# Kernel tuning notes

Hardware: AMD Instinct MI355X
Metric: run time of the kernel (lower is better)

The kernel has to match this reference:

```python
import jax, jax.numpy as jnp
import numpy as np

A = -0.75  # torch bicubic coefficient
K = 5
K2 = K * K
IN_CH = 32 * 2 + 169 + 16 * 2 + 1  # 266
TIMESTEP = 0.5


def _cubic_w(t):
    # t in [0,1); weights for taps at offsets -1,0,1,2 (torch cubic convolution, A=-0.75)
    w1 = ((A + 2.0) * t - (A + 3.0)) * t * t + 1.0
    s = 1.0 - t
    w2 = ((A + 2.0) * s - (A + 3.0)) * s * s + 1.0
    u = t + 1.0
    w0 = ((A * u - 5.0 * A) * u + 8.0 * A) * u - 4.0 * A
    v = 2.0 - t
    w3 = ((A * v - 5.0 * A) * v + 8.0 * A) * v - 4.0 * A
    return (w0, w1, w2, w3)


def _conv3(x, w, b):
    y = jax.lax.conv_general_dilated(x, w, (1, 1), 'SAME',
                                     dimension_numbers=('NCHW', 'OIHW', 'NCHW'))
    return y + b[None, :, None, None]


def _lrelu(x):
    return jnp.where(x >= 0, x, 0.1 * x)


def _kernel_pred(x, w1, b1, w2, b2, w3, b3, ow, ob, ww, wb):
    f = _lrelu(_conv3(x, w1, b1))
    f = _lrelu(_conv3(f, w2, b2))
    f = _lrelu(_conv3(f, w3, b3))
    offsets = _conv3(f, ow, ob)                      # (B, 2*K2, H, W)
    weights = jax.nn.softmax(_conv3(f, ww, wb), axis=1)  # (B, K2, H, W)
    return offsets, weights


def _adacof_sample(image, offsets, weights):
    # bicubic grid_sample(padding_mode='border', align_corners=True) + weighted combine
    b, c, h, w = image.shape
    k2 = weights.shape[1]
    gx = jnp.arange(w, dtype=image.dtype)
    gy = jnp.arange(h, dtype=image.dtype)
    dx = offsets[:, 0::2]                # (b,k2,h,w)
    dy = offsets[:, 1::2]
    # with align_corners=True, normalize->unnormalize is identity
    sx = gx[None, None, None, :] + dx
    sy = gy[None, None, :, None] + dy
    x0 = jnp.floor(sx); tx = sx - x0
    y0 = jnp.floor(sy); ty = sy - y0
    wx = _cubic_w(tx)
    wy = _cubic_w(ty)
    xi = [jnp.clip(x0 + (i - 1.0), 0, w - 1).astype(jnp.int32) for i in range(4)]
    yi = [jnp.clip(y0 + (i - 1.0), 0, h - 1).astype(jnp.int32) for i in range(4)]
    imgf = image.reshape(b, c, h * w)
    gather = jax.vmap(lambda im, idx: im[:, idx])   # (c,hw),(n,)->(c,n)
    acc = jnp.zeros((b, c, k2, h, w), image.dtype)
    for i in range(4):
        for j in range(4):
            idx = (yi[i] * w + xi[j]).reshape(b, -1)
            g = gather(imgf, idx).reshape(b, c, k2, h, w)
            acc = acc + g * (wy[i] * wx[j])[:, None]
    return jnp.einsum('bckhw,bkhw->bchw', acc, weights)


def setup_inputs() -> dict:
    key = jax.random.key(0)
    ks = iter(jax.random.split(key, 64))
    d = {}
    d['frame1'] = jax.random.normal(next(ks), (2, 3, 256, 256), jnp.float32)
    d['frame2'] = jax.random.normal(next(ks), (2, 3, 256, 256), jnp.float32)
    d['feat1'] = jax.random.normal(next(ks), (2, 32, 256, 256), jnp.float32)
    d['feat2'] = jax.random.normal(next(ks), (2, 32, 256, 256), jnp.float32)
    d['corr'] = jax.random.normal(next(ks), (2, 169, 256, 256), jnp.float32)

    def conv_w(o, i):
        return jax.random.normal(next(ks), (o, i, 3, 3), jnp.float32) * 0.05

    # full-res encoder
    d['fr_w1'] = conv_w(16, 3); d['fr_b1'] = jnp.zeros((16,), jnp.float32)
    d['fr_w2'] = conv_w(16, 16); d['fr_b2'] = jnp.zeros((16,), jnp.float32)
    # default grid offsets for offset_head bias (dx,dy interleaved)
    off_bias = []
    for i in range(K):
        for j in range(K):
            off_bias.extend([j - K // 2, i - K // 2])
    off_bias = jnp.asarray(off_bias, jnp.float32)
    for p in ('kp1', 'kp2'):
        d[p + '_w1'] = conv_w(256, IN_CH); d[p + '_b1'] = jnp.zeros((256,), jnp.float32)
        d[p + '_w2'] = conv_w(256, 256); d[p + '_b2'] = jnp.zeros((256,), jnp.float32)
        d[p + '_w3'] = conv_w(128, 256); d[p + '_b3'] = jnp.zeros((128,), jnp.float32)
        d[p + '_ow'] = jax.random.normal(next(ks), (2 * K2, 128, 3, 3), jnp.float32) * 0.01
        d[p + '_ob'] = off_bias
        d[p + '_ww'] = jax.random.normal(next(ks), (K2, 128, 3, 3), jnp.float32) * 0.01
        d[p + '_wb'] = jnp.full((K2,), 1.0 / K2, jnp.float32)
    d['bl_w1'] = conv_w(64, IN_CH); d['bl_b1'] = jnp.zeros((64,), jnp.float32)
    d['bl_w2'] = conv_w(1, 64); d['bl_b2'] = jnp.zeros((1,), jnp.float32)
    return d


def reference(frame1, frame2, feat1, feat2, corr,
              fr_w1, fr_b1, fr_w2, fr_b2,
              kp1_w1, kp1_b1, kp1_w2, kp1_b2, kp1_w3, kp1_b3, kp1_ow, kp1_ob, kp1_ww, kp1_wb,
              kp2_w1, kp2_b1, kp2_w2, kp2_b2, kp2_w3, kp2_b3, kp2_ow, kp2_ob, kp2_ww, kp2_wb,
              bl_w1, bl_b1, bl_w2, bl_b2):
    b, _, h, w = frame1.shape
    fr1 = _lrelu(_conv3(_lrelu(_conv3(frame1, fr_w1, fr_b1)), fr_w2, fr_b2))
    fr2 = _lrelu(_conv3(_lrelu(_conv3(frame2, fr_w1, fr_b1)), fr_w2, fr_b2))
    t_map = jnp.full((b, 1, h, w), TIMESTEP, frame1.dtype)
    combined = jnp.concatenate([feat1, feat2, corr, fr1, fr2, t_map], axis=1)
    offsets1, weights1 = _kernel_pred(combined, kp1_w1, kp1_b1, kp1_w2, kp1_b2,
                                      kp1_w3, kp1_b3, kp1_ow, kp1_ob, kp1_ww, kp1_wb)
    offsets2, weights2 = _kernel_pred(combined, kp2_w1, kp2_b1, kp2_w2, kp2_b2,
                                      kp2_w3, kp2_b3, kp2_ow, kp2_ob, kp2_ww, kp2_wb)
    sample1 = _adacof_sample(frame1, offsets1, weights1)
    sample2 = _adacof_sample(frame2, offsets2, weights2)
    blend = jax.nn.sigmoid(_conv3(_lrelu(_conv3(combined, bl_w1, bl_b1)), bl_w2, bl_b2))
    output = blend * sample1 + (1.0 - blend) * sample2
    return (output, blend, offsets1, offsets2, weights1, weights2)
```

## Files before the change

kernel.cpp:

```cpp
#include <hip/hip_runtime.h>
#include <cstdint>
#include <cstddef>

#define H 256
#define W 256
#define HW (H*W)
#define BATCH 2
#define CIN_TILE 4

typedef __bf16 bf16x8 __attribute__((ext_vector_type(8)));
typedef float f32x4 __attribute__((ext_vector_type(4)));
typedef __attribute__((address_space(1))) uint32_t gu32_t;
typedef __attribute__((address_space(3))) uint32_t lu32_t;

__device__ __forceinline__ void async16(const void* g, void* l) {
  __builtin_amdgcn_global_load_lds((const gu32_t*)g, (lu32_t*)l, 16, 0, 0);
}

__device__ __forceinline__ ushort f2bf(float f) {
  uint u = __float_as_uint(f);
  return (ushort)((u + 0x7FFFu + ((u >> 16) & 1u)) >> 16);
}
__device__ __forceinline__ float lrelu_f(float v) { return v >= 0.f ? v : 0.1f * v; }

template<int EPI>
__global__ __launch_bounds__(256) void convmm_k(
    const ushort* __restrict__ act, const ushort* __restrict__ wgt,
    const float* __restrict__ bias, ushort* __restrict__ dstb,
    float* __restrict__ dsto, float* __restrict__ dstw,
    const ushort* __restrict__ zpage, int Cin, int CoutS,
    int astride, int wstride, int bstride, int dstride)
{
  const int z = blockIdx.z;
  act += (size_t)z * astride;
  wgt += (size_t)z * wstride;
  bias += (size_t)z * bstride;
  if constexpr (EPI == 0) dstb += (size_t)z * dstride;
  else { dsto += (size_t)z * (BATCH * 50 * HW); dstw += (size_t)z * (BATCH * 25 * HW); }

  __shared__ __align__(16) ushort s_w[2304 * 8];
  __shared__ __align__(16) ushort s_b[1536 * 8];

  const int tid = threadIdx.x;
  const int sp = blockIdx.x;
  const int bx = (sp & 7) * 32, by = (sp >> 3) * 8;
  const int co0 = blockIdx.y * 64;
  const int wv = tid >> 6, lane = tid & 63;
  const int c = lane & 15, kq = lane >> 4;
  const int oy = wv * 2;

  int wsrc[9];
#pragma unroll
  for (int it = 0; it < 9; ++it) {
    int i = tid + it * 256;
    int co = i & 63, tk = i >> 6, tap = tk >> 2, kg = tk & 3;
    wsrc[it] = ((co0 + co) * 9 + tap) * Cin + kg * 8;
  }
  int bsrc[6];
#pragma unroll
  for (int it = 0; it < 6; ++it) {
    int i = tid + it * 256;
    int kg = i / 384, px = i - kg * 384;
    int row = px / 34, xx = px - row * 34;
    int gy = by + row - 1, gx = bx + xx - 1;
    bool ok = (px < 340) && ((unsigned)gy < (unsigned)H) && ((unsigned)gx < (unsigned)W);
    bsrc[it] = ok ? ((gy * W + gx) * Cin + kg * 8) : -1;
  }

  f32x4 acc[4][4];
#pragma unroll
  for (int a = 0; a < 4; ++a)
#pragma unroll
    for (int b2 = 0; b2 < 4; ++b2) acc[a][b2] = (f32x4){0.f, 0.f, 0.f, 0.f};

  const int nch = Cin >> 5;
  for (int ch = 0; ch < nch; ++ch) {
    const int c0 = ch << 5;
    __syncthreads();
#pragma unroll
    for (int it = 0; it < 9; ++it)
      async16(wgt + wsrc[it] + c0, &s_w[(size_t)(tid + it * 256) * 8]);
#pragma unroll
    for (int it = 0; it < 6; ++it) {
      const ushort* g = (bsrc[it] < 0) ? zpage : (act + bsrc[it] + c0);
      async16(g, &s_b[(size_t)(tid + it * 256) * 8]);
    }
    __syncthreads();

#pragma unroll
    for (int t = 0; t < 9; ++t) {
      const int dy = t / 3 - 1, dx = t % 3 - 1;
      bf16x8 B[4];
#pragma unroll
      for (int pf = 0; pf < 4; ++pf) {
        int p = (oy + (pf >> 1) + dy + 1) * 34 + (pf & 1) * 16 + dx + 1 + c;
        B[pf] = *(const bf16x8*)&s_b[(size_t)(kq * 384 + p) * 8];
      }
#pragma unroll
      for (int cf = 0; cf < 4; ++cf) {
        bf16x8 A = *(const bf16x8*)&s_w[(size_t)((t * 4 + kq) * 64 + cf * 16 + c) * 8];
#pragma unroll
        for (int pf = 0; pf < 4; ++pf)
          acc[cf][pf] = __builtin_amdgcn_mfma_f32_16x16x32_bf16(A, B[pf], acc[cf][pf], 0, 0, 0);
      }
    }
  }

  const int r4 = kq * 4;
#pragma unroll
  for (int cf = 0; cf < 4; ++cf) {
    int cob = co0 + cf * 16 + r4;
#pragma unroll
    for (int pf = 0; pf < 4; ++pf) {
      int gx2 = bx + (pf & 1) * 16 + c;
      int gy2 = by + oy + (pf >> 1);
      int gpix = gy2 * W + gx2;
      f32x4 v = acc[cf][pf];
      const float4 bv = *(const float4*)&bias[cob];
      if constexpr (EPI == 0) {
        ushort4 ov;
        float f0 = lrelu_f(v[0] + bv.x);
        float f1 = lrelu_f(v[1] + bv.y);
        float f2 = lrelu_f(v[2] + bv.z);
        float f3 = lrelu_f(v[3] + bv.w);
        ov.x = f2bf(f0); ov.y = f2bf(f1); ov.z = f2bf(f2); ov.w = f2bf(f3);
        *(ushort4*)&dstb[(size_t)gpix * CoutS + cob] = ov;
      } else {
        const float* bvp = &bv.x;
#pragma unroll
        for (int r = 0; r < 4; ++r) {
          int coa = cob + r;
          if (coa < 75) {
            float f = v[r] + bvp[r];
            if (coa < 50) dsto[(size_t)coa * HW + gpix] = f;
            else          dstw[(size_t)(coa - 50) * HW + gpix] = f;
          }
        }
      }
    }
  }
}

template<int CIN>
__global__ __launch_bounds__(256) void conv_fr_k(
    const float* __restrict__ sA, const float* __restrict__ sB, int mode,
    const float* __restrict__ wgt, const float* __restrict__ bias,
    float* __restrict__ dst)
{
  const int z = blockIdx.y;
  const float* src = (mode == 0)
      ? (((z >> 1) ? sB : sA) + (size_t)(z & 1) * 3 * HW)
      : (sA + (size_t)z * 16 * HW);
  float* out = dst + (size_t)z * 16 * HW;

  const int sp = blockIdx.x;
  const int bx = (sp & 7) * 32, by = (sp >> 3) * 32;
  const int tid = threadIdx.x;
  const int tx = tid & 15, ty = tid >> 4;

  __shared__ float s_in[CIN_TILE][34][36];
  float acc[16][2][2];
#pragma unroll
  for (int co = 0; co < 16; ++co) {
    acc[co][0][0] = 0.f; acc[co][0][1] = 0.f;
    acc[co][1][0] = 0.f; acc[co][1][1] = 0.f;
  }

  for (int c0 = 0; c0 < CIN; c0 += CIN_TILE) {
    __syncthreads();
    const int nst = CIN_TILE * 34 * 34;
    for (int i = tid; i < nst; i += 256) {
      int ci = i / (34 * 34);
      int r = i - ci * (34 * 34);
      int yy = r / 34;
      int xx = r - yy * 34;
      int gy = by + yy - 1, gx = bx + xx - 1;
      int cc = c0 + ci;
      float v = 0.f;
      if (cc < CIN && (unsigned)gy < (unsigned)H && (unsigned)gx < (unsigned)W)
        v = src[(size_t)cc * HW + gy * W + gx];
      s_in[ci][yy][xx] = v;
    }
    __syncthreads();

    const int cmax = (CIN - c0 < CIN_TILE) ? (CIN - c0) : CIN_TILE;
    for (int ci = 0; ci < cmax; ++ci) {
      float win[4][4];
#pragma unroll
      for (int iy = 0; iy < 4; ++iy)
#pragma unroll
        for (int ix = 0; ix < 4; ++ix)
          win[iy][ix] = s_in[ci][2 * ty + iy][2 * tx + ix];
#pragma unroll
      for (int co = 0; co < 16; ++co) {
        const float* wp = wgt + ((size_t)co * CIN + (c0 + ci)) * 9;
        float w0 = wp[0], w1 = wp[1], w2 = wp[2];
        float w3 = wp[3], w4 = wp[4], w5 = wp[5];
        float w6 = wp[6], w7 = wp[7], w8 = wp[8];
#pragma unroll
        for (int py = 0; py < 2; ++py)
#pragma unroll
          for (int px = 0; px < 2; ++px) {
            float s = acc[co][py][px];
            s += w0 * win[py + 0][px + 0];
            s += w1 * win[py + 0][px + 1];
            s += w2 * win[py + 0][px + 2];
            s += w3 * win[py + 1][px + 0];
            s += w4 * win[py + 1][px + 1];
            s += w5 * win[py + 1][px + 2];
            s += w6 * win[py + 2][px + 0];
            s += w7 * win[py + 2][px + 1];
            s += w8 * win[py + 2][px + 2];
            acc[co][py][px] = s;
          }
      }
    }
  }
#pragma unroll
  for (int co = 0; co < 16; ++co) {
    float bv = bias[co];
#pragma unroll
    for (int py = 0; py < 2; ++py)
#pragma unroll
      for (int px = 0; px < 2; ++px)
        out[(size_t)co * HW + (size_t)(by + 2 * ty + py) * W + (bx + 2 * tx + px)] =
            lrelu_f(acc[co][py][px] + bv);
  }
}

__global__ __launch_bounds__(256) void pack_k(
    const float* __restrict__ feat1, const float* __restrict__ feat2,
    const float* __restrict__ corr, const float* __restrict__ fr,
    ushort* __restrict__ comb, int b)
{
  int gid = blockIdx.x * 256 + threadIdx.x;
  int chunk = gid / HW;
  int p = gid - chunk * HW;
  int c0 = chunk * 32;

  uint u[16];
#pragma unroll
  for (int j = 0; j < 32; j += 2) {
    float f[2];
#pragma unroll
    for (int q = 0; q < 2; ++q) {
      int cc = c0 + j + q;
      float v;
      if (cc < 32)       v = feat1[(size_t)(b * 32 + cc) * HW + p];
      else if (cc < 64)  v = feat2[(size_t)(b * 32 + cc - 32) * HW + p];
      else if (cc < 233) v = corr[(size_t)(b * 169 + cc - 64) * HW + p];
      else if (cc < 249) v = fr[(size_t)(b * 16 + (cc - 233)) * HW + p];
      else if (cc < 265) v = fr[(size_t)((2 + b) * 16 + (cc - 249)) * HW + p];
      else if (cc == 265) v = 0.5f;
      else               v = 0.f;
      f[q] = v;
    }
    u[j >> 1] = (uint)f2bf(f[0]) | ((uint)f2bf(f[1]) << 16);
  }
  uint4* dst = (uint4*)&comb[(size_t)p * 288 + c0];
#pragma unroll
  for (int q = 0; q < 4; ++q) {
    uint4 t;
    t.x = u[q * 4 + 0]; t.y = u[q * 4 + 1]; t.z = u[q * 4 + 2]; t.w = u[q * 4 + 3];
    dst[q] = t;
  }
}

struct PrepSeg { const float* src; ushort* dst; int O, I, Ipad; };
struct PrepArgs { PrepSeg s[13]; int pre[14]; };

__global__ __launch_bounds__(256) void prep_all_k(PrepArgs a)
{
  int gid = blockIdx.x * 256 + threadIdx.x;
  if (gid >= a.pre[13]) return;
  int si = 0;
  while (gid >= a.pre[si + 1]) ++si;
  int idx = gid - a.pre[si];
  const PrepSeg sg = a.s[si];
  int i = idx % sg.Ipad;
  int r = idx / sg.Ipad;
  int tap = r % 9;
  int o = r / 9;
  float v = (i < sg.I) ? sg.src[((size_t)o * sg.I + i) * 9 + tap] : 0.f;
  sg.dst[idx] = f2bf(v);
}

__global__ __launch_bounds__(256) void bias_all_k(
    const float* kb1_0, const float* kb1_1, const float* kb2_0, const float* kb2_1,
    const float* kb3_0, const float* kb3_1,
    const float* ob0, const float* wb0, const float* ob1, const float* wb1,
    float* bb1, float* bb2, float* bb3, float* bbh)
{
  int yq = blockIdx.y;
  int i = threadIdx.x;
  switch (yq) {
    case 0: bb1[i] = kb1_0[i]; break;
    case 1: bb1[256 + i] = kb1_1[i]; break;
    case 2: bb2[i] = kb2_0[i]; break;
    case 3: bb2[256 + i] = kb2_1[i]; break;
    case 4: if (i < 128) bb3[i] = kb3_0[i]; break;
    case 5: if (i < 128) bb3[128 + i] = kb3_1[i]; break;
    case 6: if (i < 128) bbh[i]       = (i < 50) ? ob0[i] : ((i < 75) ? wb0[i - 50] : 0.f); break;
    case 7: if (i < 128) bbh[128 + i] = (i < 50) ? ob1[i] : ((i < 75) ? wb1[i - 50] : 0.f); break;
  }
}

__global__ __launch_bounds__(256) void blend2_k(
    const ushort* __restrict__ actD, const float* __restrict__ wgt,
    const float* __restrict__ b2, float* __restrict__ outp)
{
  int p = blockIdx.x * 256 + threadIdx.x;
  int y = p >> 8, x = p & 255;
  float acc = b2[0];
  for (int dy = -1; dy <= 1; ++dy) {
    int gy = y + dy;
    if ((unsigned)gy >= (unsigned)H) continue;
    for (int dx = -1; dx <= 1; ++dx) {
      int gx = x + dx;
      if ((unsigned)gx >= (unsigned)W) continue;
      int tap = (dy + 1) * 3 + (dx + 1);
      const ushort* rowp = actD + (size_t)(gy * W + gx) * 64;
#pragma unroll
      for (int c8 = 0; c8 < 8; ++c8) {
        uint4 v = *(const uint4*)&rowp[c8 * 8];
        const uint* vv = &v.x;
#pragma unroll
        for (int q = 0; q < 4; ++q) {
          float f0 = __uint_as_float(vv[q] << 16);
          float f1 = __uint_as_float(vv[q] & 0xFFFF0000u);
          int ci = c8 * 8 + q * 2;
          acc += f0 * wgt[ci * 9 + tap];
          acc += f1 * wgt[(ci + 1) * 9 + tap];
        }
      }
    }
  }
  outp[p] = 1.f / (1.f + expf(-acc));
}

__global__ __launch_bounds__(256) void softmax25_k(float* __restrict__ w1,
                                                   float* __restrict__ w2)
{
  float* wr = blockIdx.y ? w2 : w1;
  int p = blockIdx.x * 256 + threadIdx.x;
  if (p >= HW) return;
  float v[25];
  float m = -1e30f;
#pragma unroll
  for (int k = 0; k < 25; ++k) {
    v[k] = wr[(size_t)k * HW + p];
    m = fmaxf(m, v[k]);
  }
  float s = 0.f;
#pragma unroll
  for (int k = 0; k < 25; ++k) {
    v[k] = expf(v[k] - m);
    s += v[k];
  }
  float inv = 1.f / s;
#pragma unroll
  for (int k = 0; k < 25; ++k)
    wr[(size_t)k * HW + p] = v[k] * inv;
}

__device__ __forceinline__ void cubic4(float t, float* cw)
{
  const float A_ = -0.75f;
  float t2 = t * t;
  cw[1] = ((A_ + 2.f) * t - (A_ + 3.f)) * t2 + 1.f;
  float s = 1.f - t;
  cw[2] = ((A_ + 2.f) * s - (A_ + 3.f)) * (s * s) + 1.f;
  float u = t + 1.f;
  cw[0] = ((A_ * u - 5.f * A_) * u + 8.f * A_) * u - 4.f * A_;
  float v = 2.f - t;
  cw[3] = ((A_ * v - 5.f * A_) * v + 8.f * A_) * v - 4.f * A_;
}

__global__ __launch_bounds__(256) void adacof_final_k(
    const float* __restrict__ frame1, const float* __restrict__ frame2,
    const float* __restrict__ off1, const float* __restrict__ off2,
    const float* __restrict__ wt1, const float* __restrict__ wt2,
    const float* __restrict__ blend, float* __restrict__ outp)
{
  __shared__ float s_red[4][64][6];
  const int wv = threadIdx.x >> 6, lane = threadIdx.x & 63;
  const int idx = blockIdx.x * 64 + lane;
  const int b = idx / HW, p = idx - b * HW;
  const int y = p >> 8, x = p & 255;

  float a1[3] = {0.f, 0.f, 0.f};
  float a2[3] = {0.f, 0.f, 0.f};

  auto samp = [&](const float* __restrict__ img, const float* __restrict__ off,
                  const float* __restrict__ wts, float* acc) {
    for (int k = wv; k < 25; k += 4) {
      float dx = off[((size_t)b * 50 + 2 * k) * HW + p];
      float dy = off[((size_t)b * 50 + 2 * k + 1) * HW + p];
      float wk = wts[((size_t)b * 25 + k) * HW + p];
      float sx = (float)x + dx, sy = (float)y + dy;
      float x0 = floorf(sx), y0 = floorf(sy);
      float tx = sx - x0, ty = sy - y0;
      float wx[4], wy[4];
      cubic4(tx, wx);
      cubic4(ty, wy);
      int xi[4], yi[4];
#pragma unroll
      for (int i = 0; i < 4; ++i) {
        xi[i] = (int)fminf(fmaxf(x0 + (float)(i - 1), 0.f), (float)(W - 1));
        yi[i] = (int)fminf(fmaxf(y0 + (float)(i - 1), 0.f), (float)(H - 1));
      }
      const float* c0 = img + ((size_t)b * 3 + 0) * HW;
      const float* c1 = img + ((size_t)b * 3 + 1) * HW;
      const float* c2 = img + ((size_t)b * 3 + 2) * HW;
#pragma unroll
      for (int i = 0; i < 4; ++i) {
#pragma unroll
        for (int j = 0; j < 4; ++j) {
          float wf = wy[i] * wx[j] * wk;
          int q = yi[i] * W + xi[j];
          acc[0] += c0[q] * wf;
          acc[1] += c1[q] * wf;
          acc[2] += c2[q] * wf;
        }
      }
    }
  };

  samp(frame1, off1, wt1, a1);
  samp(frame2, off2, wt2, a2);

#pragma unroll
  for (int c3 = 0; c3 < 3; ++c3) {
    s_red[wv][lane][c3] = a1[c3];
    s_red[wv][lane][3 + c3] = a2[c3];
  }
  __syncthreads();
  if (wv == 0) {
    float bl = blend[(size_t)b * HW + p];
#pragma unroll
    for (int c3 = 0; c3 < 3; ++c3) {
      float r1 = s_red[0][lane][c3] + s_red[1][lane][c3] +
                 s_red[2][lane][c3] + s_red[3][lane][c3];
      float r2 = s_red[0][lane][3 + c3] + s_red[1][lane][3 + c3] +
                 s_red[2][lane][3 + c3] + s_red[3][lane][3 + c3];
      outp[((size_t)b * 3 + c3) * HW + p] = bl * r1 + (1.f - bl) * r2;
    }
  }
}

extern "C" void kernel_launch(void* const* d_in, const int* in_sizes, int n_in,
                              void* d_out, int out_size, void* d_ws, size_t ws_size,
                              hipStream_t stream)
{
  const float* frame1 = (const float*)d_in[0];
  const float* frame2 = (const float*)d_in[1];
  const float* feat1  = (const float*)d_in[2];
  const float* feat2  = (const float*)d_in[3];
  const float* corr   = (const float*)d_in[4];
  const float* fr_w1  = (const float*)d_in[5];
  const float* fr_b1  = (const float*)d_in[6];
  const float* fr_w2  = (const float*)d_in[7];
  const float* fr_b2  = (const float*)d_in[8];

  const float* kw1[2] = {(const float*)d_in[9],  (const float*)d_in[19]};
  const float* kb1[2] = {(const float*)d_in[10], (const float*)d_in[20]};
  const float* kw2[2] = {(const float*)d_in[11], (const float*)d_in[21]};
  const float* kb2[2] = {(const float*)d_in[12], (const float*)d_in[22]};
  const float* kw3[2] = {(const float*)d_in[13], (const float*)d_in[23]};
  const float* kb3[2] = {(const float*)d_in[14], (const float*)d_in[24]};
  const float* kow[2] = {(const float*)d_in[15], (const float*)d_in[25]};
  const float* kob[2] = {(const float*)d_in[16], (const float*)d_in[26]};
  const float* kww[2] = {(const float*)d_in[17], (const float*)d_in[27]};
  const float* kwb[2] = {(const float*)d_in[18], (const float*)d_in[28]};

  const float* bl_w1 = (const float*)d_in[29];
  const float* bl_b1 = (const float*)d_in[30];
  const float* bl_w2 = (const float*)d_in[31];
  const float* bl_b2 = (const float*)d_in[32];

  float* out = (float*)d_out;
  float* o_out   = out;
  float* o_blend = o_out   + (size_t)BATCH * 3 * HW;
  float* o_off1  = o_blend + (size_t)BATCH * 1 * HW;
  float* o_off2  = o_off1  + (size_t)BATCH * 50 * HW;
  float* o_w1    = o_off2  + (size_t)BATCH * 50 * HW;
  float* o_w2    = o_w1    + (size_t)BATCH * 25 * HW;

  size_t off = 0;
  char* wsb = (char*)d_ws;
  auto alloc = [&](size_t bytes) -> void* {
    void* pp = wsb + off;
    off += (bytes + 255) & ~(size_t)255;
    return pp;
  };
  const size_t NEED_MERGED = 212700000;
  const bool merged = ws_size >= NEED_MERGED;
  const int NZ = merged ? 2 : 1;

  ushort* zpage = (ushort*)alloc(512);
  ushort* wp1   = (ushort*)alloc((size_t)2 * 256 * 9 * 288 * 2);
  ushort* wp2   = (ushort*)alloc((size_t)2 * 256 * 9 * 256 * 2);
  ushort* wp3   = (ushort*)alloc((size_t)2 * 128 * 9 * 256 * 2);
  ushort* wph   = (ushort*)alloc((size_t)2 * 128 * 9 * 128 * 2);
  ushort* wpb   = (ushort*)alloc((size_t)64 * 9 * 288 * 2);
  float*  bb1   = (float*)alloc(2 * 256 * 4);
  float*  bb2   = (float*)alloc(2 * 256 * 4);
  float*  bb3   = (float*)alloc(2 * 128 * 4);
  float*  bbh   = (float*)alloc(2 * 128 * 4);
  float*  tmp4  = (float*)alloc((size_t)4 * 16 * HW * 4);
  float*  frbuf = (float*)alloc((size_t)4 * 16 * HW * 4);
  ushort* comb  = (ushort*)alloc((size_t)HW * 288 * 2);
  ushort* actA  = (ushort*)alloc((size_t)NZ * HW * 256 * 2);
  ushort* actB  = (ushort*)alloc((size_t)NZ * HW * 256 * 2);

  dim3 blk(256);

  hipMemsetAsync(zpage, 0, 512, stream);
  {
    PrepArgs pa;
    const int W1 = 256 * 9 * 288, W2 = 256 * 9 * 256, W3 = 128 * 9 * 256;
    const int OW = 50 * 9 * 128, WW = 25 * 9 * 128, ZW = 53 * 9 * 128;
    const int WB = 64 * 9 * 288;
    const int HP = 128 * 9 * 128;
    PrepSeg segs[13] = {
      {kw1[0], wp1,                    256, 266, 288},
      {kw1[1], wp1 + W1,               256, 266, 288},
      {kw2[0], wp2,                    256, 256, 256},
      {kw2[1], wp2 + W2,               256, 256, 256},
      {kw3[0], wp3,                    128, 256, 256},
      {kw3[1], wp3 + W3,               128, 256, 256},
      {kow[0], wph,                     50, 128, 128},
      {kww[0], wph + OW,                25, 128, 128},
      {nullptr, wph + OW + WW,          53,   0, 128},
      {kow[1], wph + HP,                50, 128, 128},
      {kww[1], wph + HP + OW,           25, 128, 128},
      {nullptr, wph + HP + OW + WW,     53,   0, 128},
      {bl_w1,  wpb,                     64, 266, 288},
    };
    int tots[13] = {W1, W1, W2, W2, W3, W3, OW, WW, ZW, OW, WW, ZW, WB};
    pa.pre[0] = 0;
    for (int s = 0; s < 13; ++s) { pa.s[s] = segs[s]; pa.pre[s + 1] = pa.pre[s] + tots[s]; }
    int nblk = (pa.pre[13] + 255) / 256;
    prep_all_k<<<dim3(nblk), blk, 0, stream>>>(pa);
  }
  bias_all_k<<<dim3(1, 8), blk, 0, stream>>>(kb1[0], kb1[1], kb2[0], kb2[1],
                                             kb3[0], kb3[1], kob[0], kwb[0],
                                             kob[1], kwb[1], bb1, bb2, bb3, bbh);

  conv_fr_k<3><<<dim3(64, 4), blk, 0, stream>>>(frame1, frame2, 0, fr_w1, fr_b1, tmp4);
  conv_fr_k<16><<<dim3(64, 4), blk, 0, stream>>>(tmp4, nullptr, 1, fr_w2, fr_b2, frbuf);

  const int W1 = 256 * 9 * 288, W2 = 256 * 9 * 256, W3 = 128 * 9 * 256;
  const int HP = 128 * 9 * 128;

  for (int b = 0; b < BATCH; ++b) {
    pack_k<<<dim3(9 * HW / 256), blk, 0, stream>>>(feat1, feat2, corr, frbuf, comb, b);

    for (int pp = 0; pp < 2 / NZ; ++pp) {
      const size_t po = pp;
      convmm_k<0><<<dim3(256, 4, NZ), blk, 0, stream>>>(
          comb, wp1 + po * W1, bb1 + po * 256, actA + po * (size_t)HW * 256,
          nullptr, nullptr, zpage, 288, 256, 0, W1, 256, HW * 256);
      convmm_k<0><<<dim3(256, 4, NZ), blk, 0, stream>>>(
          actA + po * (size_t)HW * 256, wp2 + po * W2, bb2 + po * 256,
          actB + po * (size_t)HW * 256,
          nullptr, nullptr, zpage, 256, 256, HW * 256, W2, 256, HW * 256);
      convmm_k<0><<<dim3(256, 2, NZ), blk, 0, stream>>>(
          actB + po * (size_t)HW * 256, wp3 + po * W3, bb3 + po * 128,
          actA + po * (size_t)HW * 128,
          nullptr, nullptr, zpage, 256, 128, HW * 256, W3, 128, HW * 128);
      convmm_k<1><<<dim3(256, 2, NZ), blk, 0, stream>>>(
          actA + po * (size_t)HW * 128, wph + po * HP, bbh + po * 128, nullptr,
          o_off1 + (size_t)b * 50 * HW + po * (size_t)BATCH * 50 * HW,
          o_w1 + (size_t)b * 25 * HW + po * (size_t)BATCH * 25 * HW,
          zpage, 128, 0, HW * 128, HP, 128, 0);
    }
    softmax25_k<<<dim3(HW / 256, 2), blk, 0, stream>>>(
        o_w1 + (size_t)b * 25 * HW, o_w2 + (size_t)b * 25 * HW);

    convmm_k<0><<<dim3(256, 1, 1), blk, 0, stream>>>(
        comb, wpb, bl_b1, actB, nullptr, nullptr, zpage, 288, 64, 0, 0, 0, 0);
    blend2_k<<<dim3(HW / 256), blk, 0, stream>>>(actB, bl_w2, bl_b2,
                                                 o_blend + (size_t)b * HW);
  }

  adacof_final_k<<<dim3(BATCH * HW / 64), blk, 0, stream>>>(
      frame1, frame2, o_off1, o_off2, o_w1, o_w2, o_blend, o_out);
}
```

Before: 1.485 ms.

## Stage image tiles with halo in LDS for AdaCoF bicubic sampling

The final AdaCoF sampling kernel now gives each block a 64x4 pixel tile. It loads a halo-padded patch of both frames into shared memory as channel-interleaved float4, and the 16-tap bicubic gathers read from LDS whenever the sampled footprint fits inside the patch, falling back to global reads otherwise. Each thread now loops over all 25 kernel taps itself, so the cross-wave shared-memory reduction and its barrier are gone. The goal is to cut scattered global gather traffic. The cost is an upfront tile load, a divergent fallback path when offsets exceed the 8-pixel halo, and less parallelism per pixel.

```diff
diff --git a/kernel.cpp b/kernel.cpp
--- a/kernel.cpp
+++ b/kernel.cpp
@@ -376,76 +376,113 @@
   cw[3] = ((A_ * v - 5.f * A_) * v + 8.f * A_) * v - 4.f * A_;
 }
 
+#define ATW 64
+#define ATH 4
+#define AHL 8
+#define AROWS (ATH + 2*AHL)
+#define ACOLS (ATW + 2*AHL)
+
 __global__ __launch_bounds__(256) void adacof_final_k(
     const float* __restrict__ frame1, const float* __restrict__ frame2,
     const float* __restrict__ off1, const float* __restrict__ off2,
     const float* __restrict__ wt1, const float* __restrict__ wt2,
     const float* __restrict__ blend, float* __restrict__ outp)
 {
-  __shared__ float s_red[4][64][6];
-  const int wv = threadIdx.x >> 6, lane = threadIdx.x & 63;
-  const int idx = blockIdx.x * 64 + lane;
-  const int b = idx / HW, p = idx - b * HW;
-  const int y = p >> 8, x = p & 255;
+  __shared__ __align__(16) float4 s_img[2 * AROWS * ACOLS];
+
+  const int tid = threadIdx.x;
+  int t = blockIdx.x;
+  const int tilesPerImg = (H / ATH) * (W / ATW);
+  const int b = t / tilesPerImg; t -= b * tilesPerImg;
+  const int by = (t >> 2) * ATH, bx = (t & 3) * ATW;
+  const int ty = tid >> 6, txx = tid & 63;
+  const int y = by + ty, x = bx + txx;
+  const int p = y * W + x;
+  const int tx0 = bx - AHL, ty0 = by - AHL;
+
+  const float* f1 = frame1 + (size_t)b * 3 * HW;
+  const float* f2 = frame2 + (size_t)b * 3 * HW;
+
+  for (int i = tid; i < AROWS * ACOLS; i += 256) {
+    int r = i / ACOLS, cc = i - r * ACOLS;
+    int gy = min(max(ty0 + r, 0), H - 1);
+    int gx = min(max(tx0 + cc, 0), W - 1);
+    int q = gy * W + gx;
+    float4 v1, v2;
+    v1.x = f1[q]; v1.y = f1[HW + q]; v1.z = f1[2 * HW + q]; v1.w = 0.f;
+    v2.x = f2[q]; v2.y = f2[HW + q]; v2.z = f2[2 * HW + q]; v2.w = 0.f;
+    s_img[i] = v1;
+    s_img[AROWS * ACOLS + i] = v2;
+  }
+  __syncthreads();
 
   float a1[3] = {0.f, 0.f, 0.f};
   float a2[3] = {0.f, 0.f, 0.f};
 
-  auto samp = [&](const float* __restrict__ img, const float* __restrict__ off,
-                  const float* __restrict__ wts, float* acc) {
-    for (int k = wv; k < 25; k += 4) {
-      float dx = off[((size_t)b * 50 + 2 * k) * HW + p];
-      float dy = off[((size_t)b * 50 + 2 * k + 1) * HW + p];
-      float wk = wts[((size_t)b * 25 + k) * HW + p];
+  const size_t ob1 = (size_t)b * 50 * HW, wb1 = (size_t)b * 25 * HW;
+
+#pragma unroll 2
+  for (int k = 0; k < 25; ++k) {
+#pragma unroll
+    for (int fr = 0; fr < 2; ++fr) {
+      const float* off = fr ? off2 : off1;
+      const float* wts = fr ? wt2 : wt1;
+      const float* img = fr ? f2 : f1;
+      float* acc = fr ? a2 : a1;
+
+      float dx = off[ob1 + (size_t)(2 * k) * HW + p];
+      float dy = off[ob1 + (size_t)(2 * k + 1) * HW + p];
+      float wk = wts[wb1 + (size_t)k * HW + p];
       float sx = (float)x + dx, sy = (float)y + dy;
-      float x0 = floorf(sx), y0 = floorf(sy);
-      float tx = sx - x0, ty = sy - y0;
+      float x0f = floorf(sx), y0f = floorf(sy);
+      float tx = sx - x0f, tyf = sy - y0f;
       float wx[4], wy[4];
       cubic4(tx, wx);
-      cubic4(ty, wy);
-      int xi[4], yi[4];
-#pragma unroll
-      for (int i = 0; i < 4; ++i) {
-        xi[i] = (int)fminf(fmaxf(x0 + (float)(i - 1), 0.f), (float)(W - 1));
-        yi[i] = (int)fminf(fmaxf(y0 + (float)(i - 1), 0.f), (float)(H - 1));
-      }
-      const float* c0 = img + ((size_t)b * 3 + 0) * HW;
-      const float* c1 = img + ((size_t)b * 3 + 1) * HW;
-      const float* c2 = img + ((size_t)b * 3 + 2) * HW;
-#pragma unroll
-      for (int i = 0; i < 4; ++i) {
-#pragma unroll
-        for (int j = 0; j < 4; ++j) {
-          float wf = wy[i] * wx[j] * wk;
-          int q = yi[i] * W + xi[j];
-          acc[0] += c0[q] * wf;
-          acc[1] += c1[q] * wf;
-          acc[2] += c2[q] * wf;
+      cubic4(tyf, wy);
+      int ix0 = (int)x0f, iy0 = (int)y0f;
+
+      bool inT = (ix0 - 1 >= tx0) && (ix0 + 2 <= tx0 + ACOLS - 1) &&
+                 (iy0 - 1 >= ty0) && (iy0 + 2 <= ty0 + AROWS - 1);
+      if (__builtin_expect(inT, 1)) {
+        const float4* base = &s_img[(size_t)fr * AROWS * ACOLS +
+                                    (iy0 - 1 - ty0) * ACOLS + (ix0 - 1 - tx0)];
+#pragma unroll
+        for (int i = 0; i < 4; ++i) {
+#pragma unroll
+          for (int j = 0; j < 4; ++j) {
+            float wf = wy[i] * wx[j] * wk;
+            float4 v = base[i * ACOLS + j];
+            acc[0] += v.x * wf;
+            acc[1] += v.y * wf;
+            acc[2] += v.z * wf;
+          }
+        }
+      } else {
+        int xi[4], yi[4];
+#pragma unroll
+        for (int i = 0; i < 4; ++i) {
+          xi[i] = min(max(ix0 + i - 1, 0), W - 1);
+          yi[i] = min(max(iy0 + i - 1, 0), H - 1);
+        }
+#pragma unroll
+        for (int i = 0; i < 4; ++i) {
+#pragma unroll
+          for (int j = 0; j < 4; ++j) {
+            float wf = wy[i] * wx[j] * wk;
+            int q = yi[i] * W + xi[j];
+            acc[0] += img[q] * wf;
+            acc[1] += img[HW + q] * wf;
+            acc[2] += img[2 * HW + q] * wf;
+          }
         }
       }
     }
-  };
-
-  samp(frame1, off1, wt1, a1);
-  samp(frame2, off2, wt2, a2);
-
-#pragma unroll
-  for (int c3 = 0; c3 < 3; ++c3) {
-    s_red[wv][lane][c3] = a1[c3];
-    s_red[wv][lane][3 + c3] = a2[c3];
-  }
-  __syncthreads();
-  if (wv == 0) {
-    float bl = blend[(size_t)b * HW + p];
-#pragma unroll
-    for (int c3 = 0; c3 < 3; ++c3) {
-      float r1 = s_red[0][lane][c3] + s_red[1][lane][c3] +
-                 s_red[2][lane][c3] + s_red[3][lane][c3];
-      float r2 = s_red[0][lane][3 + c3] + s_red[1][lane][3 + c3] +
-                 s_red[2][lane][3 + c3] + s_red[3][lane][3 + c3];
-      outp[((size_t)b * 3 + c3) * HW + p] = bl * r1 + (1.f - bl) * r2;
-    }
-  }
+  }
+
+  float bl = blend[(size_t)b * HW + p];
+#pragma unroll
+  for (int c3 = 0; c3 < 3; ++c3)
+    outp[((size_t)b * 3 + c3) * HW + p] = bl * a1[c3] + (1.f - bl) * a2[c3];
 }
 
 extern "C" void kernel_launch(void* const* d_in, const int* in_sizes, int n_in,
@@ -584,6 +621,6 @@
                                                  o_blend + (size_t)b * HW);
   }
 
-  adacof_final_k<<<dim3(BATCH * HW / 64), blk, 0, stream>>>(
+  adacof_final_k<<<dim3(BATCH * (H / ATH) * (W / ATW)), blk, 0, stream>>>(
       frame1, frame2, o_off1, o_off2, o_w1, o_w2, o_blend, o_out);
 }
```

Measured after the change: 1.304 ms. 1.14x faster.
